# Optimization experiments

Hardware: AMD Instinct MI355X
Metric: run time of the kernel (lower is better)

## Reference

```python
import jax, jax.numpy as jnp
import numpy as np

N, E, B = 50000, 100000, 512   # nodes, edges, graphs
H, F_NODE, F_EDGE, T_OUT = 64, 16, 8, 1
T = 3                           # message-passing steps


def setup_inputs() -> dict:
    key = jax.random.key(0)
    ks = jax.random.split(key, 18)

    def w(k, shape, fan_in):
        return jax.random.normal(k, shape, dtype=jnp.float32) / np.sqrt(fan_in)

    return {
        "node_features": jax.random.normal(ks[0], (N, F_NODE), dtype=jnp.float32),
        "edge_features": jax.random.normal(ks[1], (E, F_EDGE), dtype=jnp.float32),
        "Esrc": jax.random.randint(ks[2], (E,), 0, N, dtype=jnp.int32),
        "Etgt": jax.random.randint(ks[3], (E,), 0, N, dtype=jnp.int32),
        "batch": jnp.sort(jax.random.randint(ks[4], (N,), 0, B, dtype=jnp.int32)),
        # input linear: node_features -> hidden
        "Win": w(ks[5], (H, F_NODE), F_NODE),
        "bin_": jnp.zeros((H,), jnp.float32),
        # edge encoder MLP: edge_features -> hidden -> hidden*hidden
        "We1": w(ks[6], (H, F_EDGE), F_EDGE),
        "be1": jnp.zeros((H,), jnp.float32),
        "We2": w(ks[7], (H * H, H), H),
        "be2": jnp.zeros((H * H,), jnp.float32),
        # GRU cell (shared across T steps)
        "Wih": w(ks[8], (3 * H, H), H),
        "bih": jnp.zeros((3 * H,), jnp.float32),
        "Whh": w(ks[9], (3 * H, H), H),
        "bhh": jnp.zeros((3 * H,), jnp.float32),
        # output linear: hidden -> target_features
        "Wout": w(ks[10], (T_OUT, H), H),
        "bout": jnp.zeros((T_OUT,), jnp.float32),
    }


def _gru(x, h, Wih, bih, Whh, bhh):
    gi = x @ Wih.T + bih            # [N, 3H]
    gh = h @ Whh.T + bhh
    i_r, i_z, i_n = jnp.split(gi, 3, axis=-1)
    h_r, h_z, h_n = jnp.split(gh, 3, axis=-1)
    r = jax.nn.sigmoid(i_r + h_r)
    z = jax.nn.sigmoid(i_z + h_z)
    n = jnp.tanh(i_n + r * h_n)
    return (1.0 - z) * n + z * h


def reference(node_features, edge_features, Esrc, Etgt, batch,
              Win, bin_, We1, be1, We2, be2,
              Wih, bih, Whh, bhh, Wout, bout):
    # Edge encoder MLP -> per-edge [H, H] message matrix (ENN style)
    eh = jax.nn.relu(edge_features @ We1.T + be1)          # [E, H]
    edge_data = (eh @ We2.T + be2).reshape(E, H, H)        # [E, H, H]

    x = node_features @ Win.T + bin_                       # [N, H]

    for _ in range(T):  # small fixed layer count
        msg = jnp.einsum('eij,ej->ei', edge_data, x[Esrc])  # per-edge matvec
        agg = jax.ops.segment_sum(msg, Etgt, num_segments=N)
        x = _gru(agg, x, Wih, bih, Whh, bhh)

    out = x @ Wout.T + bout                                # [N, 1]
    pooled = jax.ops.segment_sum(out, batch, num_segments=B)  # [B, 1]
    return pooled
```

## Files before the change

### kernel.cpp

```cpp
#include <hip/hip_runtime.h>
#include <hip/hip_fp16.h>

#define NN 50000
#define NE 100000
#define NB 512

typedef _Float16 f16x8 __attribute__((ext_vector_type(8)));
typedef float f32x4  __attribute__((ext_vector_type(4)));

__device__ __forceinline__ float sigm(float v) { return 1.0f / (1.0f + __expf(-v)); }
__device__ __forceinline__ float tanh_fast(float v) {
    float e = __expf(-2.0f * fabsf(v));
    float t = (1.0f - e) / (1.0f + e);
    return v < 0.f ? -t : t;
}

__global__ __launch_bounds__(256) void node_in_kernel(
    const float* __restrict__ nf, const float* __restrict__ Win,
    const float* __restrict__ bin_, float* __restrict__ x, __half* __restrict__ xh)
{
    int idx = blockIdx.x * 256 + threadIdx.x;
    if (idx >= NN * 64) return;
    int n = idx >> 6, h = idx & 63;
    float acc = bin_[h];
    #pragma unroll
    for (int f = 0; f < 16; f++) acc += nf[n * 16 + f] * Win[h * 16 + f];
    x[idx] = acc;
    xh[idx] = __float2half(acc);
}

__global__ __launch_bounds__(256) void edge_l1_kernel(
    const float* __restrict__ ef, const float* __restrict__ We1,
    const float* __restrict__ be1, __half* __restrict__ ehh)
{
    int idx = blockIdx.x * 256 + threadIdx.x;
    if (idx >= NE * 64) return;
    int e = idx >> 6, k = idx & 63;
    float acc = be1[k];
    #pragma unroll
    for (int f = 0; f < 8; f++) acc += ef[e * 8 + f] * We1[k * 8 + f];
    ehh[idx] = __float2half(fmaxf(acc, 0.0f));
}

__global__ __launch_bounds__(256) void pack_b_kernel(
    const float* __restrict__ We2, const float* __restrict__ be2,
    __half* __restrict__ Bp)
{
    int idx = blockIdx.x * 256 + threadIdx.x;
    if (idx >= 130 * 64 * 32) return;
    int kk = idx & 31;
    int n  = (idx >> 5) & 63;
    int kt = idx >> 11;
    int p  = kt * 32 + kk;
    float v;
    if (p < 4096) {
        int j = p >> 6, k = p & 63;
        v = We2[((size_t)(n * 64 + j)) * 64 + k];
    } else {
        v = be2[n * 64 + (p - 4096)];
    }
    Bp[idx] = __float2half(v);
}

__global__ __launch_bounds__(256) void pack_gru_kernel(
    const float* __restrict__ Wih, const float* __restrict__ Whh,
    __half* __restrict__ WG)
{
    int idx = blockIdx.x * 256 + threadIdx.x;
    if (idx >= 24576) return;
    int kk = idx & 31;
    int n  = (idx >> 5) & 15;
    int nt = (idx >> 9) % 24;
    int kt = (idx >> 9) / 24;
    int k = kt * 32 + kk;
    int col192 = (nt % 12) * 16 + n;
    int gate = col192 >> 6, h = col192 & 63;
    const float* src = (nt < 12) ? Wih : Whh;
    WG[idx] = __float2half(src[((size_t)(gate * 64 + h)) * 64 + k]);
}

__global__ __launch_bounds__(256, 3) void msg_kernel(
    const __half* __restrict__ xh, const __half* __restrict__ ehh,
    const __half* __restrict__ Bp,
    const int* __restrict__ Esrc, const int* __restrict__ Etgt,
    float* __restrict__ agg)
{
    __shared__ __half xs[4][64][72];
    __shared__ int tgt_s[256];
    const int tid = threadIdx.x;
    const int e0 = blockIdx.x * 256;
    const int w = tid >> 6, lane = tid & 63;

    {
        const int e = e0 + tid;
        const bool ok = (e < NE);
        const int src = ok ? Esrc[e] : 0;
        tgt_s[tid] = ok ? Etgt[e] : -1;
        const uint4* xsrc = (const uint4*)(xh + (size_t)src * 64);
        #pragma unroll
        for (int i = 0; i < 8; i++) {
            uint4 v = ok ? xsrc[i] : make_uint4(0, 0, 0, 0);
            *(uint4*)(&xs[w][lane][i * 8]) = v;
        }
    }
    __syncthreads();

    const int m = lane & 15;
    const int quad = lane >> 4;

    __half2 ehc2[4][2][4];
    #pragma unroll
    for (int mt = 0; mt < 4; mt++) {
        const int e = e0 + w * 64 + mt * 16 + m;
        if (e < NE) {
            union { uint4 u; __half2 h[4]; } u0, u1;
            u0.u = *(const uint4*)(ehh + (size_t)e * 64 + quad * 8);
            u1.u = *(const uint4*)(ehh + (size_t)e * 64 + 32 + quad * 8);
            #pragma unroll
            for (int q = 0; q < 4; q++) { ehc2[mt][0][q] = u0.h[q]; ehc2[mt][1][q] = u1.h[q]; }
        } else {
            __half2 z = __halves2half2(__float2half(0.f), __float2half(0.f));
            #pragma unroll
            for (int q = 0; q < 4; q++) { ehc2[mt][0][q] = z; ehc2[mt][1][q] = z; }
        }
    }

    f32x4 acc[4][4];
    #pragma unroll
    for (int a = 0; a < 4; a++)
        #pragma unroll
        for (int b = 0; b < 4; b++)
            #pragma unroll
            for (int q = 0; q < 4; q++) acc[a][b][q] = 0.f;

    const __half* blane = Bp + m * 32 + quad * 8;

    #pragma unroll 1
    for (int j = 0; j < 64; j++) {
        __half2 xsj2[4];
        #pragma unroll
        for (int mt = 0; mt < 4; mt++) {
            __half v = xs[w][mt * 16 + m][j];
            xsj2[mt] = __halves2half2(v, v);
        }
        #pragma unroll
        for (int half = 0; half < 2; half++) {
            const int kt = 2 * j + half;
            f16x8 bfrag[4];
            #pragma unroll
            for (int nt = 0; nt < 4; nt++)
                bfrag[nt] = *(const f16x8*)(blane + (size_t)kt * 2048 + nt * 512);
            #pragma unroll
            for (int mt = 0; mt < 4; mt++) {
                union { __half2 h[4]; f16x8 v; } u;
                #pragma unroll
                for (int q = 0; q < 4; q++)
                    u.h[q] = __hmul2(xsj2[mt], ehc2[mt][half][q]);
                #pragma unroll
                for (int nt = 0; nt < 4; nt++)
                    acc[mt][nt] = __builtin_amdgcn_mfma_f32_16x16x32_f16(
                        u.v, bfrag[nt], acc[mt][nt], 0, 0, 0);
            }
        }
    }

    #pragma unroll
    for (int half = 0; half < 2; half++) {
        const int kt = 128 + half;
        f16x8 bfrag[4];
        #pragma unroll
        for (int nt = 0; nt < 4; nt++)
            bfrag[nt] = *(const f16x8*)(blane + (size_t)kt * 2048 + nt * 512);
        #pragma unroll
        for (int mt = 0; mt < 4; mt++) {
            f16x8 af = *(const f16x8*)(&xs[w][mt * 16 + m][half * 32 + quad * 8]);
            #pragma unroll
            for (int nt = 0; nt < 4; nt++)
                acc[mt][nt] = __builtin_amdgcn_mfma_f32_16x16x32_f16(
                    af, bfrag[nt], acc[mt][nt], 0, 0, 0);
        }
    }

    #pragma unroll
    for (int mt = 0; mt < 4; mt++) {
        #pragma unroll
        for (int r = 0; r < 4; r++) {
            const int row = w * 64 + mt * 16 + quad * 4 + r;
            const int t = tgt_s[row];
            if (t >= 0) {
                #pragma unroll
                for (int nt = 0; nt < 4; nt++)
                    atomicAdd(agg + (size_t)t * 64 + nt * 16 + m, acc[mt][nt][r]);
            }
        }
    }
}

__global__ __launch_bounds__(256, 3) void gru_kernel(
    const float* __restrict__ agg, float* __restrict__ x, __half* __restrict__ xh,
    const __half* __restrict__ WG,
    const float* __restrict__ bih, const float* __restrict__ bhh)
{
    __shared__ __half wlds[24576];
    const int tid = threadIdx.x;
    {
        const uint4* src = (const uint4*)WG;
        uint4* dst = (uint4*)wlds;
        #pragma unroll
        for (int i = 0; i < 12; i++) dst[i * 256 + tid] = src[i * 256 + tid];
    }
    __syncthreads();

    const int w = tid >> 6, lane = tid & 63, m = lane & 15, quad = lane >> 4;
    const int nbase = blockIdx.x * 64 + w * 16;
    const int anode = nbase + m;
    const bool aok = (anode < NN);

    f16x8 a_agg[2], a_x[2];
    #pragma unroll
    for (int kt = 0; kt < 2; kt++) {
        const int koff = kt * 32 + quad * 8;
        if (aok) {
            const float* ap = agg + (size_t)anode * 64 + koff;
            float4 f0 = *(const float4*)ap;
            float4 f1 = *(const float4*)(ap + 4);
            union { __half2 h[4]; f16x8 v; } u;
            u.h[0] = __floats2half2_rn(f0.x, f0.y);
            u.h[1] = __floats2half2_rn(f0.z, f0.w);
            u.h[2] = __floats2half2_rn(f1.x, f1.y);
            u.h[3] = __floats2half2_rn(f1.z, f1.w);
            a_agg[kt] = u.v;
            a_x[kt] = *(const f16x8*)(xh + (size_t)anode * 64 + koff);
        } else {
            f16x8 z;
            #pragma unroll
            for (int i = 0; i < 8; i++) z[i] = (_Float16)0;
            a_agg[kt] = z; a_x[kt] = z;
        }
    }

    f32x4 acc[24];
    #pragma unroll
    for (int nt = 0; nt < 24; nt++)
        #pragma unroll
        for (int q = 0; q < 4; q++) acc[nt][q] = 0.f;

    #pragma unroll
    for (int kt = 0; kt < 2; kt++) {
        #pragma unroll
        for (int nt = 0; nt < 24; nt++) {
            f16x8 b = *(const f16x8*)(wlds + (kt * 24 + nt) * 512 + m * 32 + quad * 8);
            acc[nt] = __builtin_amdgcn_mfma_f32_16x16x32_f16(
                (nt < 12) ? a_agg[kt] : a_x[kt], b, acc[nt], 0, 0, 0);
        }
    }

    #pragma unroll
    for (int t = 0; t < 4; t++) {
        const int h = t * 16 + m;
        const float bir = bih[h], biz = bih[64 + h], bin = bih[128 + h];
        const float bhr = bhh[h], bhz = bhh[64 + h], bhn = bhh[128 + h];
        #pragma unroll
        for (int r = 0; r < 4; r++) {
            const int nd = nbase + quad * 4 + r;
            if (nd >= NN) continue;
            float ir  = acc[t][r]      + bir;
            float iz  = acc[4 + t][r]  + biz;
            float in_ = acc[8 + t][r]  + bin;
            float hr  = acc[12 + t][r] + bhr;
            float hz  = acc[16 + t][r] + bhz;
            float hn  = acc[20 + t][r] + bhn;
            float rg = sigm(ir + hr);
            float z  = sigm(iz + hz);
            float n  = tanh_fast(in_ + rg * hn);
            float xold = x[(size_t)nd * 64 + h];
            float xn = (1.0f - z) * n + z * xold;
            x[(size_t)nd * 64 + h] = xn;
            xh[(size_t)nd * 64 + h] = __float2half(xn);
        }
    }
}

__global__ __launch_bounds__(256) void pool_kernel(
    const float* __restrict__ x, const float* __restrict__ Wout,
    const float* __restrict__ bout, const int* __restrict__ batch,
    float* __restrict__ out)
{
    const int node = blockIdx.x * 256 + threadIdx.x;
    if (node >= NN) return;
    float acc = bout[0];
    const float4* xp = (const float4*)(x + (size_t)node * 64);
    #pragma unroll
    for (int i = 0; i < 16; i++) {
        float4 v = xp[i];
        acc += v.x * Wout[4*i] + v.y * Wout[4*i+1] + v.z * Wout[4*i+2] + v.w * Wout[4*i+3];
    }
    atomicAdd(out + batch[node], acc);
}

extern "C" void kernel_launch(void* const* d_in, const int* in_sizes, int n_in,
                              void* d_out, int out_size, void* d_ws, size_t ws_size,
                              hipStream_t stream)
{
    const float* nf   = (const float*)d_in[0];
    const float* ef   = (const float*)d_in[1];
    const int*   Esrc = (const int*)  d_in[2];
    const int*   Etgt = (const int*)  d_in[3];
    const int*   bat  = (const int*)  d_in[4];
    const float* Win  = (const float*)d_in[5];
    const float* bin_ = (const float*)d_in[6];
    const float* We1  = (const float*)d_in[7];
    const float* be1  = (const float*)d_in[8];
    const float* We2  = (const float*)d_in[9];
    const float* be2  = (const float*)d_in[10];
    const float* Wih  = (const float*)d_in[11];
    const float* bih  = (const float*)d_in[12];
    const float* Whh  = (const float*)d_in[13];
    const float* bhh  = (const float*)d_in[14];
    const float* Wout = (const float*)d_in[15];
    const float* bout = (const float*)d_in[16];

    char* ws = (char*)d_ws;
    float*  x   = (float*)(ws);
    float*  agg = (float*)(ws + 12800000);
    __half* xh  = (__half*)(ws + 25600000);
    __half* ehh = (__half*)(ws + 32000000);
    __half* Bp  = (__half*)(ws + 44800000);
    __half* WG  = (__half*)(ws + 45400064);

    hipMemsetAsync(d_out, 0, NB * sizeof(float), stream);

    node_in_kernel<<<(NN * 64 + 255) / 256, 256, 0, stream>>>(nf, Win, bin_, x, xh);
    edge_l1_kernel<<<(NE * 64 + 255) / 256, 256, 0, stream>>>(ef, We1, be1, ehh);
    pack_b_kernel<<<(130 * 64 * 32 + 255) / 256, 256, 0, stream>>>(We2, be2, Bp);
    pack_gru_kernel<<<(24576 + 255) / 256, 256, 0, stream>>>(Wih, Whh, WG);

    for (int t = 0; t < 3; t++) {
        hipMemsetAsync(agg, 0, (size_t)NN * 64 * sizeof(float), stream);
        msg_kernel<<<(NE + 255) / 256, 256, 0, stream>>>(xh, ehh, Bp, Esrc, Etgt, agg);
        gru_kernel<<<(NN + 63) / 64, 256, 0, stream>>>(agg, x, xh, WG, bih, bhh);
    }

    pool_kernel<<<(NN + 255) / 256, 256, 0, stream>>>(x, Wout, bout, bat, (float*)d_out);
}
```

Before: 479.8 us.

## Stage packed edge-weight B tiles through double-buffered LDS in msg kernel

The message kernel now cooperatively loads each 4096-half slab of the packed We2 matrix into a double-buffered shared-memory tile, prefetching the next slab into registers while computing on the current one. It also halves edges per block (128 instead of 256, two 16-row tiles per wave) and repacks Bp so each lane reads contiguous 8-half fragments. The goal is to stop every wave from reading B fragments separately from global memory and to overlap those loads with MFMA work. In exchange it adds a block-wide barrier each iteration, reads B from global twice as often in total because there are twice as many blocks, and uses more LDS, which may reduce occupancy.

```diff
diff --git a/kernel.cpp b/kernel.cpp
--- a/kernel.cpp
+++ b/kernel.cpp
@@ -47,10 +47,13 @@
     __half* __restrict__ Bp)
 {
     int idx = blockIdx.x * 256 + threadIdx.x;
-    if (idx >= 130 * 64 * 32) return;
-    int kk = idx & 31;
-    int n  = (idx >> 5) & 63;
+    if (idx >= 130 * 2048) return;
+    int i  = idx & 7;
+    int l  = (idx >> 3) & 63;
+    int nt = (idx >> 9) & 3;
     int kt = idx >> 11;
+    int n  = nt * 16 + (l & 15);
+    int kk = (l >> 4) * 8 + i;
     int p  = kt * 32 + kk;
     float v;
     if (p < 4096) {
@@ -85,33 +88,40 @@
     const int* __restrict__ Esrc, const int* __restrict__ Etgt,
     float* __restrict__ agg)
 {
-    __shared__ __half xs[4][64][72];
-    __shared__ int tgt_s[256];
+    __shared__ __half xs[4][32][72];
+    __shared__ __half bbuf[2][4096];
+    __shared__ int tgt_s[128];
     const int tid = threadIdx.x;
-    const int e0 = blockIdx.x * 256;
+    const int e0 = blockIdx.x * 128;
     const int w = tid >> 6, lane = tid & 63;
+    const int m = lane & 15, quad = lane >> 4;
 
     {
-        const int e = e0 + tid;
+        const int r = tid >> 1, part = tid & 1;
+        const int e = e0 + r;
         const bool ok = (e < NE);
         const int src = ok ? Esrc[e] : 0;
-        tgt_s[tid] = ok ? Etgt[e] : -1;
-        const uint4* xsrc = (const uint4*)(xh + (size_t)src * 64);
-        #pragma unroll
-        for (int i = 0; i < 8; i++) {
+        if (part == 0) tgt_s[r] = ok ? Etgt[e] : -1;
+        const uint4* xsrc = (const uint4*)(xh + (size_t)src * 64 + part * 32);
+        __half* dst = &xs[r >> 5][r & 31][part * 32];
+        #pragma unroll
+        for (int i = 0; i < 4; i++) {
             uint4 v = ok ? xsrc[i] : make_uint4(0, 0, 0, 0);
-            *(uint4*)(&xs[w][lane][i * 8]) = v;
-        }
-    }
-    __syncthreads();
-
-    const int m = lane & 15;
-    const int quad = lane >> 4;
-
-    __half2 ehc2[4][2][4];
-    #pragma unroll
-    for (int mt = 0; mt < 4; mt++) {
-        const int e = e0 + w * 64 + mt * 16 + m;
+            *(uint4*)(dst + i * 8) = v;
+        }
+    }
+
+    {
+        const uint4* s = (const uint4*)Bp;
+        uint4 v0 = s[tid], v1 = s[256 + tid];
+        ((uint4*)bbuf[0])[tid] = v0;
+        ((uint4*)bbuf[0])[256 + tid] = v1;
+    }
+
+    __half2 ehc2[2][2][4];
+    #pragma unroll
+    for (int mt = 0; mt < 2; mt++) {
+        const int e = e0 + w * 32 + mt * 16 + m;
         if (e < NE) {
             union { uint4 u; __half2 h[4]; } u0, u1;
             u0.u = *(const uint4*)(ehh + (size_t)e * 64 + quad * 8);
@@ -125,33 +135,37 @@
         }
     }
 
-    f32x4 acc[4][4];
-    #pragma unroll
-    for (int a = 0; a < 4; a++)
+    f32x4 acc[2][4];
+    #pragma unroll
+    for (int a = 0; a < 2; a++)
         #pragma unroll
         for (int b = 0; b < 4; b++)
             #pragma unroll
             for (int q = 0; q < 4; q++) acc[a][b][q] = 0.f;
 
-    const __half* blane = Bp + m * 32 + quad * 8;
-
+    __syncthreads();
+
+    int cur = 0;
     #pragma unroll 1
     for (int j = 0; j < 64; j++) {
-        __half2 xsj2[4];
-        #pragma unroll
-        for (int mt = 0; mt < 4; mt++) {
+        const uint4* s = (const uint4*)(Bp + (size_t)(j + 1) * 4096);
+        uint4 p0 = s[tid];
+        uint4 p1 = s[256 + tid];
+
+        __half2 xsj2[2];
+        #pragma unroll
+        for (int mt = 0; mt < 2; mt++) {
             __half v = xs[w][mt * 16 + m][j];
             xsj2[mt] = __halves2half2(v, v);
         }
         #pragma unroll
         for (int half = 0; half < 2; half++) {
-            const int kt = 2 * j + half;
-            f16x8 bfrag[4];
+            f16x8 bf[4];
             #pragma unroll
             for (int nt = 0; nt < 4; nt++)
-                bfrag[nt] = *(const f16x8*)(blane + (size_t)kt * 2048 + nt * 512);
-            #pragma unroll
-            for (int mt = 0; mt < 4; mt++) {
+                bf[nt] = *(const f16x8*)(&bbuf[cur][half * 2048 + nt * 512 + lane * 8]);
+            #pragma unroll
+            for (int mt = 0; mt < 2; mt++) {
                 union { __half2 h[4]; f16x8 v; } u;
                 #pragma unroll
                 for (int q = 0; q < 4; q++)
@@ -159,33 +173,38 @@
                 #pragma unroll
                 for (int nt = 0; nt < 4; nt++)
                     acc[mt][nt] = __builtin_amdgcn_mfma_f32_16x16x32_f16(
-                        u.v, bfrag[nt], acc[mt][nt], 0, 0, 0);
+                        u.v, bf[nt], acc[mt][nt], 0, 0, 0);
             }
         }
+
+        uint4* d = (uint4*)bbuf[cur ^ 1];
+        d[tid] = p0;
+        d[256 + tid] = p1;
+        __syncthreads();
+        cur ^= 1;
     }
 
     #pragma unroll
     for (int half = 0; half < 2; half++) {
-        const int kt = 128 + half;
-        f16x8 bfrag[4];
+        f16x8 bf[4];
         #pragma unroll
         for (int nt = 0; nt < 4; nt++)
-            bfrag[nt] = *(const f16x8*)(blane + (size_t)kt * 2048 + nt * 512);
-        #pragma unroll
-        for (int mt = 0; mt < 4; mt++) {
+            bf[nt] = *(const f16x8*)(&bbuf[cur][half * 2048 + nt * 512 + lane * 8]);
+        #pragma unroll
+        for (int mt = 0; mt < 2; mt++) {
             f16x8 af = *(const f16x8*)(&xs[w][mt * 16 + m][half * 32 + quad * 8]);
             #pragma unroll
             for (int nt = 0; nt < 4; nt++)
                 acc[mt][nt] = __builtin_amdgcn_mfma_f32_16x16x32_f16(
-                    af, bfrag[nt], acc[mt][nt], 0, 0, 0);
-        }
-    }
-
-    #pragma unroll
-    for (int mt = 0; mt < 4; mt++) {
+                    af, bf[nt], acc[mt][nt], 0, 0, 0);
+        }
+    }
+
+    #pragma unroll
+    for (int mt = 0; mt < 2; mt++) {
         #pragma unroll
         for (int r = 0; r < 4; r++) {
-            const int row = w * 64 + mt * 16 + quad * 4 + r;
+            const int row = w * 32 + mt * 16 + quad * 4 + r;
             const int t = tgt_s[row];
             if (t >= 0) {
                 #pragma unroll
@@ -332,12 +351,12 @@
 
     node_in_kernel<<<(NN * 64 + 255) / 256, 256, 0, stream>>>(nf, Win, bin_, x, xh);
     edge_l1_kernel<<<(NE * 64 + 255) / 256, 256, 0, stream>>>(ef, We1, be1, ehh);
-    pack_b_kernel<<<(130 * 64 * 32 + 255) / 256, 256, 0, stream>>>(We2, be2, Bp);
+    pack_b_kernel<<<(130 * 2048 + 255) / 256, 256, 0, stream>>>(We2, be2, Bp);
     pack_gru_kernel<<<(24576 + 255) / 256, 256, 0, stream>>>(Wih, Whh, WG);
 
     for (int t = 0; t < 3; t++) {
         hipMemsetAsync(agg, 0, (size_t)NN * 64 * sizeof(float), stream);
-        msg_kernel<<<(NE + 255) / 256, 256, 0, stream>>>(xh, ehh, Bp, Esrc, Etgt, agg);
+        msg_kernel<<<(NE + 127) / 128, 256, 0, stream>>>(xh, ehh, Bp, Esrc, Etgt, agg);
         gru_kernel<<<(NN + 63) / 64, 256, 0, stream>>>(agg, x, xh, WG, bih, bhh);
     }
 
```

After: 472.5 us. Within noise of the previous version (-1.5%).
